# Optimization experiments

Hardware: AMD Instinct MI355X
Metric: run time of the kernel (lower is better)

## Reference

```python
import math
import jax, jax.numpy as jnp
import numpy as np

B, H, T, D = 1, 16, 2048, 64
DIM = H * D
WINDOW = 256  # sliding window size


def sliding_window_mask(seq_len, window):
    # token i attends to tokens max(0, i-window+1) .. i
    row = jnp.arange(seq_len)[:, None]
    col = jnp.arange(seq_len)[None, :]
    return (col <= row) & (col > row - window)


def setup_inputs() -> dict:
    key = jax.random.key(0)
    kq, kk, kv, kw = jax.random.split(key, 4)
    q = jax.random.normal(kq, (B, H, T, D), dtype=jnp.float32)
    k = jax.random.normal(kk, (B, H, T, D), dtype=jnp.float32)
    v = jax.random.normal(kv, (B, H, T, D), dtype=jnp.float32)
    W_proj = jax.random.normal(kw, (DIM, DIM), dtype=jnp.float32) * (1.0 / math.sqrt(DIM))
    return {"q": q, "k": k, "v": v, "W_proj": W_proj}


def reference(q, k, v, W_proj):
    b, h, t, d = q.shape
    scale = 1.0 / math.sqrt(d)
    mask = sliding_window_mask(t, WINDOW)  # (T, T) bool
    # scaled dot-product attention logits: (B, H, T, T)
    att = jnp.einsum("bhqd,bhkd->bhqk", q, k) * scale
    att = jnp.where(mask, att, jnp.finfo(att.dtype).min)
    att = jax.nn.softmax(att, axis=-1)
    y = jnp.einsum("bhqk,bhkd->bhqd", att, v)  # (B, H, T, D)
    y = y.transpose(0, 2, 1, 3).reshape(b, t, h * d)  # (B, T, dim)
    return y @ W_proj  # c_proj, no bias
```

## Files before the change

kernel.cpp:

```cpp
#include <hip/hip_runtime.h>

#define T_SEQ 2048
#define NH    16
#define HD    64
#define DIM   1024
#define WIN   256

typedef __attribute__((ext_vector_type(4))) float f32x4;
typedef __attribute__((ext_vector_type(8))) short s16x8;
typedef unsigned short u16;

static __device__ __forceinline__ u16 f2bf(float f) {
    unsigned u = __builtin_bit_cast(unsigned, f);
    u += 0x7fff + ((u >> 16) & 1);
    return (u16)(u >> 16);
}

static __device__ __forceinline__ int fV(int d) { return (d & 7) ^ ((d >> 3) & 7); }

static __device__ __forceinline__ void gload16(const void* g, void* l) {
    __builtin_amdgcn_global_load_lds(
        (const __attribute__((address_space(1))) unsigned int*)g,
        (__attribute__((address_space(3))) unsigned int*)l, 16, 0, 0);
}

__global__ __launch_bounds__(256) void prep_kernel(const float* __restrict__ W,
                                                   u16* __restrict__ Wt,
                                                   const float* __restrict__ qg,
                                                   const float* __restrict__ kg,
                                                   const float* __restrict__ vg,
                                                   u16* __restrict__ y) {
    __shared__ __align__(16) char smem[4 * 16 * 128 + 2 * 64 * 128];
    const int bid = (int)blockIdx.x;
    const int t   = threadIdx.x;

    if (bid < 256) {
        float(*sT)[69] = (float(*)[69])smem;
        const int k0 = (bid & 15) * 64;
        const int n0 = (bid >> 4) * 64;
#pragma unroll
        for (int i = 0; i < 4; ++i) {
            const int idx = i * 256 + t;
            const int kr = idx >> 4, c4 = (idx & 15) * 4;
            float4 v = *(const float4*)(W + (size_t)(k0 + kr) * DIM + n0 + c4);
            sT[kr][c4] = v.x; sT[kr][c4 + 1] = v.y; sT[kr][c4 + 2] = v.z; sT[kr][c4 + 3] = v.w;
        }
        __syncthreads();
#pragma unroll
        for (int i = 0; i < 2; ++i) {
            const int idx = i * 256 + t;
            const int nr = idx >> 3, ch = (idx & 7) * 8;
            s16x8 o;
#pragma unroll
            for (int e = 0; e < 8; ++e) o[e] = f2bf(sT[ch + e][nr]);
            *(s16x8*)(Wt + (size_t)(n0 + nr) * DIM + k0 + ch) = o;
        }
        return;
    }

    char* sK  = smem;
    char* sV  = smem + 64 * 128;
    char* sPb = smem + 2 * 64 * 128;

    const int ab   = bid - 256;
    const int swzb = (ab & 7) * 64 + (ab >> 3);
    const int lane = t & 63;
    const int w    = t >> 6;
    const int q0   = (swzb & 31) * 64;
    const int h    = swzb >> 5;
    const size_t headBase = (size_t)h * T_SEQ * HD;

    const int lr = lane & 15;
    const int lg = lane >> 4;

    s16x8 qf[2];
    {
        const float* qrow = qg + headBase + (size_t)(q0 + w * 16 + lr) * HD + lg * 8;
#pragma unroll
        for (int s = 0; s < 2; ++s) {
            float4 a = *(const float4*)(qrow + 32 * s);
            float4 b = *(const float4*)(qrow + 32 * s + 4);
            s16x8 f;
            f[0] = f2bf(a.x); f[1] = f2bf(a.y); f[2] = f2bf(a.z); f[3] = f2bf(a.w);
            f[4] = f2bf(b.x); f[5] = f2bf(b.y); f[6] = f2bf(b.z); f[7] = f2bf(b.w);
            qf[s] = f;
        }
    }

    f32x4 o[4];
#pragma unroll
    for (int i = 0; i < 4; ++i) o[i] = (f32x4){0.f, 0.f, 0.f, 0.f};
    float lsum[4] = {0.f, 0.f, 0.f, 0.f};

    int lo = q0 - (WIN - 1);
    if (lo < 0) lo = 0;
    const int kc0 = lo & ~63;

    const int srow = t >> 2;
    const int sd0  = (t & 3) * 16;

    for (int kc = kc0; kc <= q0; kc += 64) {
        __syncthreads();
        {
            const float* ksrc = kg + headBase + (size_t)(kc + srow) * HD + sd0;
            float4 k0 = *(const float4*)(ksrc);
            float4 k1 = *(const float4*)(ksrc + 4);
            float4 k2 = *(const float4*)(ksrc + 8);
            float4 k3 = *(const float4*)(ksrc + 12);
            s16x8 c0, c1;
            c0[0] = f2bf(k0.x); c0[1] = f2bf(k0.y); c0[2] = f2bf(k0.z); c0[3] = f2bf(k0.w);
            c0[4] = f2bf(k1.x); c0[5] = f2bf(k1.y); c0[6] = f2bf(k1.z); c0[7] = f2bf(k1.w);
            c1[0] = f2bf(k2.x); c1[1] = f2bf(k2.y); c1[2] = f2bf(k2.z); c1[3] = f2bf(k2.w);
            c1[4] = f2bf(k3.x); c1[5] = f2bf(k3.y); c1[6] = f2bf(k3.z); c1[7] = f2bf(k3.w);
            const int swz = (srow & 7) << 4;
            *(s16x8*)(sK + srow * 128 + ((sd0 * 2) ^ swz))      = c0;
            *(s16x8*)(sK + srow * 128 + ((sd0 * 2 + 16) ^ swz)) = c1;

            const float* vsrc = vg + headBase + (size_t)(kc + srow) * HD + sd0;
            float4 v0 = *(const float4*)(vsrc);
            float4 v1 = *(const float4*)(vsrc + 4);
            float4 v2 = *(const float4*)(vsrc + 8);
            float4 v3 = *(const float4*)(vsrc + 12);
            float vv[16] = {v0.x, v0.y, v0.z, v0.w, v1.x, v1.y, v1.z, v1.w,
                            v2.x, v2.y, v2.z, v2.w, v3.x, v3.y, v3.z, v3.w};
#pragma unroll
            for (int e = 0; e < 16; ++e) {
                const int d = sd0 + e;
                *(u16*)(sV + d * 128 + ((srow * 2) ^ (fV(d) << 4))) = f2bf(vv[e]);
            }
        }
        __syncthreads();

        char* pw = sPb + w * 16 * 128;
#pragma unroll
        for (int kt = 0; kt < 4; ++kt) {
            const int krow = kt * 16 + lr;
            const int kswz = (krow & 7) << 4;
            s16x8 kf0 = *(const s16x8*)(sK + krow * 128 + ((lg * 16) ^ kswz));
            s16x8 kf1 = *(const s16x8*)(sK + krow * 128 + ((lg * 16 + 64) ^ kswz));
            f32x4 s = (f32x4){0.f, 0.f, 0.f, 0.f};
            s = __builtin_amdgcn_mfma_f32_16x16x32_bf16(qf[0], kf0, s, 0, 0, 0);
            s = __builtin_amdgcn_mfma_f32_16x16x32_bf16(qf[1], kf1, s, 0, 0, 0);
            const int key = kc + kt * 16 + lr;
#pragma unroll
            for (int r = 0; r < 4; ++r) {
                const int qrow = q0 + w * 16 + lg * 4 + r;
                float pv = 0.f;
                if (key <= qrow && key > qrow - WIN) pv = __expf(s[r] * 0.125f);
                lsum[r] += pv;
                const int prow = lg * 4 + r;
                *(u16*)(pw + prow * 128 + ((kt * 32 + lr * 2) ^ ((prow & 7) << 4))) = f2bf(pv);
            }
        }

        s16x8 pf0 = *(const s16x8*)(pw + lr * 128 + ((lg * 16) ^ ((lr & 7) << 4)));
        s16x8 pf1 = *(const s16x8*)(pw + lr * 128 + ((lg * 16 + 64) ^ ((lr & 7) << 4)));
#pragma unroll
        for (int td = 0; td < 4; ++td) {
            const int drow = td * 16 + lr;
            const int vswz = fV(drow) << 4;
            s16x8 vf0 = *(const s16x8*)(sV + drow * 128 + ((lg * 16) ^ vswz));
            s16x8 vf1 = *(const s16x8*)(sV + drow * 128 + ((lg * 16 + 64) ^ vswz));
            o[td] = __builtin_amdgcn_mfma_f32_16x16x32_bf16(pf0, vf0, o[td], 0, 0, 0);
            o[td] = __builtin_amdgcn_mfma_f32_16x16x32_bf16(pf1, vf1, o[td], 0, 0, 0);
        }
    }

#pragma unroll
    for (int m = 1; m < 16; m <<= 1) {
#pragma unroll
        for (int r = 0; r < 4; ++r) lsum[r] += __shfl_xor(lsum[r], m, 64);
    }
    float rl[4];
#pragma unroll
    for (int r = 0; r < 4; ++r) rl[r] = 1.f / lsum[r];
#pragma unroll
    for (int td = 0; td < 4; ++td)
#pragma unroll
        for (int r = 0; r < 4; ++r)
            y[(size_t)(q0 + w * 16 + lg * 4 + r) * DIM + h * HD + td * 16 + lr] =
                f2bf(o[td][r] * rl[r]);
}

__global__ __launch_bounds__(256) void proj_kernel(const u16* __restrict__ A,
                                                   const u16* __restrict__ Bt,
                                                   float* __restrict__ out) {
    __shared__ __align__(16) char sA[3][128 * 128];
    __shared__ __align__(16) char sB[3][64 * 128];

    const int t    = threadIdx.x;
    const int lane = t & 63;
    const int w    = t >> 6;
    const int wr   = w >> 1, wc = w & 1;
    const int lr   = lane & 15, lg = lane >> 4;

    const int id   = (int)blockIdx.x;
    const int wgid = (id & 7) * 32 + (id >> 3);
    const int m0   = (wgid >> 4) * 128;
    const int n0   = (wgid & 15) * 64;

    f32x4 acc[4][2];
#pragma unroll
    for (int i = 0; i < 4; ++i)
#pragma unroll
        for (int j = 0; j < 2; ++j) acc[i][j] = (f32x4){0.f, 0.f, 0.f, 0.f};

    const int sRow = lane >> 3;
    const int sCh  = lane & 7;

#define STAGE(buf, k0)                                                                 \
    do {                                                                               \
        _Pragma("unroll") for (int p = 0; p < 4; ++p) {                                \
            const int pi  = p * 4 + w;                                                 \
            const int row = pi * 8 + sRow;                                             \
            gload16(A + (size_t)(m0 + row) * DIM + (k0) + ((sCh ^ (row & 7)) << 3),    \
                    sA[buf] + pi * 1024);                                              \
        }                                                                              \
        _Pragma("unroll") for (int p = 0; p < 2; ++p) {                                \
            const int pi  = p * 4 + w;                                                 \
            const int row = pi * 8 + sRow;                                             \
            gload16(Bt + (size_t)(n0 + row) * DIM + (k0) + ((sCh ^ (row & 7)) << 3),   \
                    sB[buf] + pi * 1024);                                              \
        }                                                                              \
    } while (0)

    STAGE(0, 0);
    STAGE(1, 64);

#pragma unroll
    for (int kt = 0; kt < DIM / 64; ++kt) {
        const int cur  = kt % 3;
        const int nxt  = (kt + 2) % 3;
        const int knxt = ((kt + 2) & 15) * 64;

        STAGE(nxt, knxt);
        asm volatile("s_waitcnt vmcnt(12)" ::: "memory");
        __builtin_amdgcn_s_barrier();

        s16x8 af[2][4], bfr[2][2];
#pragma unroll
        for (int kh = 0; kh < 2; ++kh) {
#pragma unroll
            for (int mi = 0; mi < 4; ++mi) {
                const int row = wr * 64 + mi * 16 + lr;
                const int cc  = kh * 4 + lg;
                af[kh][mi] = *(const s16x8*)(sA[cur] + row * 128 + ((cc ^ (row & 7)) << 4));
            }
#pragma unroll
            for (int ni = 0; ni < 2; ++ni) {
                const int row = wc * 32 + ni * 16 + lr;
                const int cc  = kh * 4 + lg;
                bfr[kh][ni] = *(const s16x8*)(sB[cur] + row * 128 + ((cc ^ (row & 7)) << 4));
            }
        }
        __builtin_amdgcn_s_setprio(1);
#pragma unroll
        for (int kh = 0; kh < 2; ++kh)
#pragma unroll
            for (int mi = 0; mi < 4; ++mi)
#pragma unroll
                for (int ni = 0; ni < 2; ++ni)
                    acc[mi][ni] = __builtin_amdgcn_mfma_f32_16x16x32_bf16(
                        af[kh][mi], bfr[kh][ni], acc[mi][ni], 0, 0, 0);
        __builtin_amdgcn_s_setprio(0);
        __builtin_amdgcn_s_barrier();
    }
#undef STAGE

    asm volatile("s_waitcnt vmcnt(0)" ::: "memory");

#pragma unroll
    for (int mi = 0; mi < 4; ++mi)
#pragma unroll
        for (int ni = 0; ni < 2; ++ni)
#pragma unroll
            for (int r = 0; r < 4; ++r)
                out[(size_t)(m0 + wr * 64 + mi * 16 + lg * 4 + r) * DIM +
                    n0 + wc * 32 + ni * 16 + lr] = acc[mi][ni][r];
}

extern "C" void kernel_launch(void* const* d_in, const int* in_sizes, int n_in,
                              void* d_out, int out_size, void* d_ws, size_t ws_size,
                              hipStream_t stream) {
    const float* q = (const float*)d_in[0];
    const float* k = (const float*)d_in[1];
    const float* v = (const float*)d_in[2];
    const float* W = (const float*)d_in[3];
    float* out = (float*)d_out;
    u16* y_bf = (u16*)d_ws;
    u16* Wt   = (u16*)d_ws + (size_t)T_SEQ * DIM;

    prep_kernel<<<768, 256, 0, stream>>>(W, Wt, q, k, v, y_bf);
    proj_kernel<<<256, 256, 0, stream>>>(y_bf, Wt, out);
}
```

Before: 37.58 us.

## Precompute bf16 K and transposed V, double-buffer attention tiles via async LDS loads

K is converted to bf16 and V to bf16 transposed in a separate conversion kernel, alongside the W transpose. A new attention kernel then streams K/V chunks into double-buffered LDS with global_load_lds and waitcnt-based pipelining instead of converting them inside the loop. This removes redundant per-block fp32→bf16 conversion, since each K/V chunk was converted by up to 5 blocks. It also overlaps the next chunk's load with current compute, at the cost of an extra kernel launch and an extra workspace round trip for K and V.

```diff
diff --git a/kernel.cpp b/kernel.cpp
--- a/kernel.cpp
+++ b/kernel.cpp
@@ -24,18 +24,17 @@
         (__attribute__((address_space(3))) unsigned int*)l, 16, 0, 0);
 }
 
-__global__ __launch_bounds__(256) void prep_kernel(const float* __restrict__ W,
+__global__ __launch_bounds__(256) void conv_kernel(const float* __restrict__ W,
                                                    u16* __restrict__ Wt,
-                                                   const float* __restrict__ qg,
                                                    const float* __restrict__ kg,
+                                                   u16* __restrict__ Kc,
                                                    const float* __restrict__ vg,
-                                                   u16* __restrict__ y) {
-    __shared__ __align__(16) char smem[4 * 16 * 128 + 2 * 64 * 128];
+                                                   u16* __restrict__ Vt) {
+    __shared__ float sT[64][69];
     const int bid = (int)blockIdx.x;
     const int t   = threadIdx.x;
 
     if (bid < 256) {
-        float(*sT)[69] = (float(*)[69])smem;
         const int k0 = (bid & 15) * 64;
         const int n0 = (bid >> 4) * 64;
 #pragma unroll
@@ -55,27 +54,70 @@
             for (int e = 0; e < 8; ++e) o[e] = f2bf(sT[ch + e][nr]);
             *(s16x8*)(Wt + (size_t)(n0 + nr) * DIM + k0 + ch) = o;
         }
-        return;
-    }
-
-    char* sK  = smem;
-    char* sV  = smem + 64 * 128;
-    char* sPb = smem + 2 * 64 * 128;
-
-    const int ab   = bid - 256;
+    } else if (bid < 768) {
+        const int vt  = bid - 256;
+        const int h   = vt >> 5;
+        const int kt0 = (vt & 31) * 64;
+        const float* src = vg + ((size_t)h * T_SEQ + kt0) * HD;
+#pragma unroll
+        for (int i = 0; i < 4; ++i) {
+            const int idx = i * 256 + t;
+            const int kr = idx >> 4, c4 = (idx & 15) * 4;
+            float4 v = *(const float4*)(src + (size_t)kr * HD + c4);
+            sT[kr][c4] = v.x; sT[kr][c4 + 1] = v.y; sT[kr][c4 + 2] = v.z; sT[kr][c4 + 3] = v.w;
+        }
+        __syncthreads();
+#pragma unroll
+        for (int i = 0; i < 2; ++i) {
+            const int idx = i * 256 + t;
+            const int nr = idx >> 3, ch = (idx & 7) * 8;
+            s16x8 o;
+#pragma unroll
+            for (int e = 0; e < 8; ++e) o[e] = f2bf(sT[ch + e][nr]);
+            *(s16x8*)(Vt + ((size_t)h * HD + nr) * T_SEQ + kt0 + ch) = o;
+        }
+    } else {
+        const int kb = bid - 768;
+        const float* src = kg + (size_t)kb * 8192;
+        u16* dst = Kc + (size_t)kb * 8192;
+#pragma unroll
+        for (int i = 0; i < 4; ++i) {
+            const int off = i * 2048 + t * 8;
+            float4 a = *(const float4*)(src + off);
+            float4 b = *(const float4*)(src + off + 4);
+            s16x8 o;
+            o[0] = f2bf(a.x); o[1] = f2bf(a.y); o[2] = f2bf(a.z); o[3] = f2bf(a.w);
+            o[4] = f2bf(b.x); o[5] = f2bf(b.y); o[6] = f2bf(b.z); o[7] = f2bf(b.w);
+            *(s16x8*)(dst + off) = o;
+        }
+    }
+}
+
+__global__ __launch_bounds__(256) void attn_kernel(const float* __restrict__ qg,
+                                                   const u16* __restrict__ Kc,
+                                                   const u16* __restrict__ Vt,
+                                                   u16* __restrict__ y) {
+    __shared__ __align__(16) char sK[2][8192];
+    __shared__ __align__(16) char sV[2][8192];
+    __shared__ __align__(16) char sP[4][2048];
+
+    const int ab   = (int)blockIdx.x;
     const int swzb = (ab & 7) * 64 + (ab >> 3);
+    const int t    = threadIdx.x;
     const int lane = t & 63;
     const int w    = t >> 6;
     const int q0   = (swzb & 31) * 64;
     const int h    = swzb >> 5;
-    const size_t headBase = (size_t)h * T_SEQ * HD;
+
+    const u16* Kh = Kc + (size_t)h * T_SEQ * HD;
+    const u16* Vh = Vt + (size_t)h * HD * T_SEQ;
 
     const int lr = lane & 15;
     const int lg = lane >> 4;
 
     s16x8 qf[2];
     {
-        const float* qrow = qg + headBase + (size_t)(q0 + w * 16 + lr) * HD + lg * 8;
+        const float* qrow = qg + ((size_t)h * T_SEQ + q0 + w * 16 + lr) * HD + lg * 8;
 #pragma unroll
         for (int s = 0; s < 2; ++s) {
             float4 a = *(const float4*)(qrow + 32 * s);
@@ -95,49 +137,43 @@
     int lo = q0 - (WIN - 1);
     if (lo < 0) lo = 0;
     const int kc0 = lo & ~63;
-
-    const int srow = t >> 2;
-    const int sd0  = (t & 3) * 16;
-
-    for (int kc = kc0; kc <= q0; kc += 64) {
-        __syncthreads();
-        {
-            const float* ksrc = kg + headBase + (size_t)(kc + srow) * HD + sd0;
-            float4 k0 = *(const float4*)(ksrc);
-            float4 k1 = *(const float4*)(ksrc + 4);
-            float4 k2 = *(const float4*)(ksrc + 8);
-            float4 k3 = *(const float4*)(ksrc + 12);
-            s16x8 c0, c1;
-            c0[0] = f2bf(k0.x); c0[1] = f2bf(k0.y); c0[2] = f2bf(k0.z); c0[3] = f2bf(k0.w);
-            c0[4] = f2bf(k1.x); c0[5] = f2bf(k1.y); c0[6] = f2bf(k1.z); c0[7] = f2bf(k1.w);
-            c1[0] = f2bf(k2.x); c1[1] = f2bf(k2.y); c1[2] = f2bf(k2.z); c1[3] = f2bf(k2.w);
-            c1[4] = f2bf(k3.x); c1[5] = f2bf(k3.y); c1[6] = f2bf(k3.z); c1[7] = f2bf(k3.w);
-            const int swz = (srow & 7) << 4;
-            *(s16x8*)(sK + srow * 128 + ((sd0 * 2) ^ swz))      = c0;
-            *(s16x8*)(sK + srow * 128 + ((sd0 * 2 + 16) ^ swz)) = c1;
-
-            const float* vsrc = vg + headBase + (size_t)(kc + srow) * HD + sd0;
-            float4 v0 = *(const float4*)(vsrc);
-            float4 v1 = *(const float4*)(vsrc + 4);
-            float4 v2 = *(const float4*)(vsrc + 8);
-            float4 v3 = *(const float4*)(vsrc + 12);
-            float vv[16] = {v0.x, v0.y, v0.z, v0.w, v1.x, v1.y, v1.z, v1.w,
-                            v2.x, v2.y, v2.z, v2.w, v3.x, v3.y, v3.z, v3.w};
-#pragma unroll
-            for (int e = 0; e < 16; ++e) {
-                const int d = sd0 + e;
-                *(u16*)(sV + d * 128 + ((srow * 2) ^ (fV(d) << 4))) = f2bf(vv[e]);
-            }
-        }
-        __syncthreads();
-
-        char* pw = sPb + w * 16 * 128;
+    const int nc  = (q0 - kc0) / 64 + 1;
+
+    const int sRow8 = lane >> 3;
+    const int sCh   = lane & 7;
+
+#define STAGE(buf, kc)                                                              \
+    do {                                                                            \
+        _Pragma("unroll") for (int j = 0; j < 2; ++j) {                             \
+            const int s_  = j * 4 + w;                                              \
+            const int row = s_ * 8 + sRow8;                                         \
+            gload16(Kh + (size_t)((kc) + row) * HD + ((sCh ^ (row & 7)) << 3),      \
+                    sK[buf] + s_ * 1024);                                           \
+            gload16(Vh + (size_t)row * T_SEQ + (kc) + ((sCh ^ fV(row)) << 3),       \
+                    sV[buf] + s_ * 1024);                                           \
+        }                                                                           \
+    } while (0)
+
+    STAGE(0, kc0);
+
+    for (int ic = 0; ic < nc; ++ic) {
+        const int kc = kc0 + ic * 64;
+        const int cb = ic & 1;
+        if (ic + 1 < nc) {
+            STAGE(cb ^ 1, kc + 64);
+            asm volatile("s_waitcnt vmcnt(4)" ::: "memory");
+        } else {
+            asm volatile("s_waitcnt vmcnt(0)" ::: "memory");
+        }
+        __builtin_amdgcn_s_barrier();
+
+        char* pw = sP[w];
 #pragma unroll
         for (int kt = 0; kt < 4; ++kt) {
             const int krow = kt * 16 + lr;
             const int kswz = (krow & 7) << 4;
-            s16x8 kf0 = *(const s16x8*)(sK + krow * 128 + ((lg * 16) ^ kswz));
-            s16x8 kf1 = *(const s16x8*)(sK + krow * 128 + ((lg * 16 + 64) ^ kswz));
+            s16x8 kf0 = *(const s16x8*)(sK[cb] + krow * 128 + ((lg * 16) ^ kswz));
+            s16x8 kf1 = *(const s16x8*)(sK[cb] + krow * 128 + ((lg * 16 + 64) ^ kswz));
             f32x4 s = (f32x4){0.f, 0.f, 0.f, 0.f};
             s = __builtin_amdgcn_mfma_f32_16x16x32_bf16(qf[0], kf0, s, 0, 0, 0);
             s = __builtin_amdgcn_mfma_f32_16x16x32_bf16(qf[1], kf1, s, 0, 0, 0);
@@ -159,12 +195,14 @@
         for (int td = 0; td < 4; ++td) {
             const int drow = td * 16 + lr;
             const int vswz = fV(drow) << 4;
-            s16x8 vf0 = *(const s16x8*)(sV + drow * 128 + ((lg * 16) ^ vswz));
-            s16x8 vf1 = *(const s16x8*)(sV + drow * 128 + ((lg * 16 + 64) ^ vswz));
+            s16x8 vf0 = *(const s16x8*)(sV[cb] + drow * 128 + ((lg * 16) ^ vswz));
+            s16x8 vf1 = *(const s16x8*)(sV[cb] + drow * 128 + ((lg * 16 + 64) ^ vswz));
             o[td] = __builtin_amdgcn_mfma_f32_16x16x32_bf16(pf0, vf0, o[td], 0, 0, 0);
             o[td] = __builtin_amdgcn_mfma_f32_16x16x32_bf16(pf1, vf1, o[td], 0, 0, 0);
         }
-    }
+        __builtin_amdgcn_s_barrier();
+    }
+#undef STAGE
 
 #pragma unroll
     for (int m = 1; m < 16; m <<= 1) {
@@ -287,9 +325,13 @@
     const float* v = (const float*)d_in[2];
     const float* W = (const float*)d_in[3];
     float* out = (float*)d_out;
+
     u16* y_bf = (u16*)d_ws;
-    u16* Wt   = (u16*)d_ws + (size_t)T_SEQ * DIM;
-
-    prep_kernel<<<768, 256, 0, stream>>>(W, Wt, q, k, v, y_bf);
+    u16* Wt   = y_bf + (size_t)T_SEQ * DIM;
+    u16* Kc   = Wt + (size_t)DIM * DIM;
+    u16* Vt   = Kc + (size_t)NH * T_SEQ * HD;
+
+    conv_kernel<<<1024, 256, 0, stream>>>(W, Wt, k, Kc, v, Vt);
+    attn_kernel<<<512, 256, 0, stream>>>(q, Kc, Vt, y_bf);
     proj_kernel<<<256, 256, 0, stream>>>(y_bf, Wt, out);
 }
```

New measurement: 38.32 us. Within noise of the previous version (+2.0%).
